# Kernel tuning notes

Hardware: AMD Instinct MI355X
Metric: run time of the kernel (lower is better)

The kernel has to match this reference:

```python
import jax, jax.numpy as jnp
from jax import lax
import numpy as np

V, H, D, B, W = 256, 512, 2, 256, 256  # vector_size, hidden_size, depth, batch, window_size


def setup_inputs() -> dict:
    key = jax.random.key(0)
    ks = jax.random.split(key, 13)
    scale = 0.04  # ~ 1/sqrt(hidden)
    names = ["w_ih_ltr", "w_hh_ltr", "b_ih_ltr", "b_hh_ltr", "w_fc_ltr", "b_fc_ltr",
             "w_ih_rtl", "w_hh_rtl", "b_ih_rtl", "b_hh_rtl", "w_fc_rtl", "b_fc_rtl"]
    shapes = [(D, 4 * H, V), (D, 4 * H, H), (D, 4 * H), (D, 4 * H), (D, V, H), (D, V)] * 2
    inp = {"x": jax.random.normal(ks[0], (B, W, V), dtype=jnp.float32)}
    for i, (n, s) in enumerate(zip(names, shapes)):
        inp[n] = jax.random.normal(ks[i + 1], s, dtype=jnp.float32) * scale
    return inp


def _lstm_cell(x, h, c, wih, whh, bih, bhh):
    # PyTorch gate order: i, f, g, o
    g = x @ wih.T + bih + h @ whh.T + bhh
    i, f, gg, o = jnp.split(g, 4, axis=-1)
    c = jax.nn.sigmoid(f) * c + jax.nn.sigmoid(i) * jnp.tanh(gg)
    h = jax.nn.sigmoid(o) * jnp.tanh(c)
    return h, c


def _run_dir(xs, wih, whh, bih, bhh, wfc, bfc):
    # xs: (T, B, V); depth LSTM(1-step)+FC blocks with persistent (h,c) per depth
    depth = wih.shape[0]
    h0 = jnp.zeros((depth, xs.shape[1], whh.shape[-1]), xs.dtype)

    def step(carry, x):
        h, c = carry
        v = x
        hs, cs = [], []
        for j in range(depth):  # small fixed depth loop
            hj, cj = _lstm_cell(v, h[j], c[j], wih[j], whh[j], bih[j], bhh[j])
            v = hj @ wfc[j].T + bfc[j]
            hs.append(hj)
            cs.append(cj)
        return (jnp.stack(hs), jnp.stack(cs)), v

    _, ys = lax.scan(step, (h0, h0), xs)
    return ys  # (T, B, V)


def reference(x, w_ih_ltr, w_hh_ltr, b_ih_ltr, b_hh_ltr, w_fc_ltr, b_fc_ltr,
              w_ih_rtl, w_hh_rtl, b_ih_rtl, b_hh_rtl, w_fc_rtl, b_fc_rtl):
    Wlen = x.shape[1]
    xs_f = jnp.swapaxes(x[:, :Wlen - 1, :], 0, 1)        # steps i = 0 .. W-2
    xs_b = jnp.swapaxes(x[:, Wlen - 1:0:-1, :], 0, 1)    # steps -(i+1) = W-1 .. 1
    ys_f = _run_dir(xs_f, w_ih_ltr, w_hh_ltr, b_ih_ltr, b_hh_ltr, w_fc_ltr, b_fc_ltr)
    ys_b = _run_dir(xs_b, w_ih_rtl, w_hh_rtl, b_ih_rtl, b_hh_rtl, w_fc_rtl, b_fc_rtl)
    # torch.stack(output, dim=1): forward outputs then backward outputs -> (B, 2*(W-1), V)
    return jnp.swapaxes(jnp.concatenate([ys_f, ys_b], axis=0), 0, 1)
```

## Files before the change

kernel.cpp:

```cpp
#include <hip/hip_runtime.h>
#include <hip/hip_bf16.h>

using bf16   = __bf16;
using bf16x8 = __attribute__((ext_vector_type(8))) __bf16;
using f32x4  = __attribute__((ext_vector_type(4))) float;
using u32x4  = __attribute__((ext_vector_type(4))) unsigned int;

#define TSTEPS 255
#define UNITE  512
#define HPAR   (16*16*512)
#define WA_UNITS_DIR (128*24)
#define WB_UNITS_DIR (128*32)
#define WC_UNITS_DIR (16*16)

#define MFMA(acc, a, b) acc = __builtin_amdgcn_mfma_f32_16x16x32_bf16((a), (b), (acc), 0, 0, 0)

__device__ __forceinline__ float sigmoidf_(float x) { return 1.f / (1.f + __expf(-x)); }
__device__ __forceinline__ float tanhf_(float x) {
    float e = __expf(-2.f * fabsf(x));
    float t = (1.f - e) / (1.f + e);
    return copysignf(t, x);
}

__device__ __forceinline__ void storeh_coh(bf16* ph, bf16* pl,
                                           unsigned short vh, unsigned short vl) {
    asm volatile(
        "global_store_short %0, %2, off sc0 sc1\n\t"
        "global_store_short %1, %3, off sc0 sc1"
        :: "v"(ph), "v"(pl), "v"(vh), "v"(vl)
        : "memory");
}

__device__ __forceinline__ void stage32k(const bf16* gh, const bf16* gl,
                                         bf16* lds, int tid) {
    u32x4 a0, a1, a2, a3, b0, b1, b2, b3;
    const bf16* p0 = gh + tid * 8;
    const bf16* p1 = p0 + 2048;
    const bf16* p2 = p0 + 4096;
    const bf16* p3 = p0 + 6144;
    const bf16* q0 = gl + tid * 8;
    const bf16* q1 = q0 + 2048;
    const bf16* q2 = q0 + 4096;
    const bf16* q3 = q0 + 6144;
    asm volatile(
        "global_load_dwordx4 %0, %8, off sc0 sc1\n\t"
        "global_load_dwordx4 %1, %9, off sc0 sc1\n\t"
        "global_load_dwordx4 %2, %10, off sc0 sc1\n\t"
        "global_load_dwordx4 %3, %11, off sc0 sc1\n\t"
        "global_load_dwordx4 %4, %12, off sc0 sc1\n\t"
        "global_load_dwordx4 %5, %13, off sc0 sc1\n\t"
        "global_load_dwordx4 %6, %14, off sc0 sc1\n\t"
        "global_load_dwordx4 %7, %15, off sc0 sc1\n\t"
        "s_waitcnt vmcnt(0)"
        : "=&v"(a0), "=&v"(a1), "=&v"(a2), "=&v"(a3),
          "=&v"(b0), "=&v"(b1), "=&v"(b2), "=&v"(b3)
        : "v"(p0), "v"(p1), "v"(p2), "v"(p3),
          "v"(q0), "v"(q1), "v"(q2), "v"(q3)
        : "memory");
    *(u32x4*)(lds + tid * 8)                 = a0;
    *(u32x4*)(lds + tid * 8 + 2048)          = a1;
    *(u32x4*)(lds + tid * 8 + 4096)          = a2;
    *(u32x4*)(lds + tid * 8 + 6144)          = a3;
    *(u32x4*)(lds + 8192 + tid * 8)          = b0;
    *(u32x4*)(lds + 8192 + tid * 8 + 2048)   = b1;
    *(u32x4*)(lds + 8192 + tid * 8 + 4096)   = b2;
    *(u32x4*)(lds + 8192 + tid * 8 + 6144)   = b3;
}

__device__ __forceinline__ void split_store8(const float* __restrict__ src,
                                             bf16* __restrict__ dh, bf16* __restrict__ dl) {
    float f[8];
    *(float4*)f       = *(const float4*)src;
    *(float4*)(f + 4) = *(const float4*)(src + 4);
    bf16x8 oh, ol;
    #pragma unroll
    for (int j = 0; j < 8; ++j) { bf16 h = (bf16)f[j]; oh[j] = h; ol[j] = (bf16)(f[j] - (float)h); }
    *(bf16x8*)dh = oh; *(bf16x8*)dl = ol;
}

__device__ __forceinline__ void gbarrier(unsigned* __restrict__ flags, int bid, unsigned epoch) {
    asm volatile("s_waitcnt vmcnt(0)" ::: "memory");
    __syncthreads();
    if (threadIdx.x == 0)
        asm volatile("global_store_dword %0, %1, off sc0 sc1"
                     :: "v"(&flags[bid]), "v"(epoch) : "memory");
    if (threadIdx.x < 64) {
        const int l = threadIdx.x;
        for (;;) {
            unsigned f0 = __hip_atomic_load(&flags[l],       __ATOMIC_RELAXED, __HIP_MEMORY_SCOPE_AGENT);
            unsigned f1 = __hip_atomic_load(&flags[l + 64],  __ATOMIC_RELAXED, __HIP_MEMORY_SCOPE_AGENT);
            unsigned f2 = __hip_atomic_load(&flags[l + 128], __ATOMIC_RELAXED, __HIP_MEMORY_SCOPE_AGENT);
            unsigned f3 = __hip_atomic_load(&flags[l + 192], __ATOMIC_RELAXED, __HIP_MEMORY_SCOPE_AGENT);
            if (__all(f0 >= epoch && f1 >= epoch && f2 >= epoch && f3 >= epoch)) break;
            __builtin_amdgcn_s_sleep(1);
        }
    }
    __syncthreads();
}


__global__ void k_pack_wa(const float* __restrict__ wihL, const float* __restrict__ whhL,
                          const float* __restrict__ wihR, const float* __restrict__ whhR,
                          bf16* __restrict__ wah, bf16* __restrict__ wal) {
    int gid = blockIdx.x * 256 + threadIdx.x;
    int lane = gid & 63, u = gid >> 6;
    int kb = u % 24; int tn = (u / 24) & 127; int dir = u / 3072;
    int r = lane & 15, q = lane >> 4;
    int n = tn * 16 + r, k = kb * 32 + q * 8;
    const float* wih = dir ? wihR : wihL;
    const float* whh = dir ? whhR : whhL;
    const float* src = (k < 256) ? (wih + (size_t)n * 256 + k)
                                 : (whh + (size_t)n * 512 + (k - 256));
    split_store8(src, wah + (size_t)u * UNITE + lane * 8, wal + (size_t)u * UNITE + lane * 8);
}

__global__ void k_wcomb(const float* __restrict__ wihL, const float* __restrict__ wfcL,
                        const float* __restrict__ wihR, const float* __restrict__ wfcR,
                        float* __restrict__ wcf) {
    size_t gid = (size_t)blockIdx.x * 256 + threadIdx.x;
    int k = gid & 511; int n = (gid >> 9) & 2047; int dir = (int)(gid >> 20);
    const float* wih1 = (dir ? wihR : wihL) + (size_t)2048 * 256;
    const float* wfc0 = (dir ? wfcR : wfcL);
    float s = 0.f;
    #pragma unroll 8
    for (int v = 0; v < 256; ++v)
        s = fmaf(wih1[(size_t)n * 256 + v], wfc0[(size_t)v * 512 + k], s);
    wcf[gid] = s;
}

__global__ void k_pack_wb(const float* __restrict__ whhL, const float* __restrict__ whhR,
                          const float* __restrict__ wcf,
                          bf16* __restrict__ wbh, bf16* __restrict__ wbl) {
    int gid = blockIdx.x * 256 + threadIdx.x;
    int lane = gid & 63, u = gid >> 6;
    int kb = u & 31, tn = (u >> 5) & 127, dir = u >> 12;
    int r = lane & 15, q = lane >> 4;
    int n = tn * 16 + r, k = kb * 32 + q * 8;
    const float* src;
    if (k < 512) {
        src = wcf + ((size_t)dir * 2048 + n) * 512 + k;
    } else {
        const float* whh1 = (dir ? whhR : whhL) + (size_t)2048 * 512;
        src = whh1 + (size_t)n * 512 + (k - 512);
    }
    split_store8(src, wbh + (size_t)u * UNITE + lane * 8, wbl + (size_t)u * UNITE + lane * 8);
}

__global__ void k_pack_wc(const float* __restrict__ wfcL, const float* __restrict__ wfcR,
                          bf16* __restrict__ wch, bf16* __restrict__ wcl) {
    int gid = blockIdx.x * 256 + threadIdx.x;
    int lane = gid & 63, u = gid >> 6;
    int kb = u & 15, tn = (u >> 4) & 15, dir = u >> 8;
    int r = lane & 15, q = lane >> 4;
    int n = tn * 16 + r, k = kb * 32 + q * 8;
    const float* wfc1 = (dir ? wfcR : wfcL) + (size_t)256 * 512;
    split_store8(wfc1 + (size_t)n * 512 + k,
                 wch + (size_t)u * UNITE + lane * 8, wcl + (size_t)u * UNITE + lane * 8);
}

__global__ void k_bias(const float* __restrict__ bihL, const float* __restrict__ bhhL,
                       const float* __restrict__ bfcL, const float* __restrict__ wihL,
                       const float* __restrict__ bihR, const float* __restrict__ bhhR,
                       const float* __restrict__ bfcR, const float* __restrict__ wihR,
                       float* __restrict__ ba, float* __restrict__ bb, float* __restrict__ bc) {
    int gid = blockIdx.x * 256 + threadIdx.x;
    int n = gid & 2047, dir = gid >> 11;
    const float* bih = dir ? bihR : bihL;
    const float* bhh = dir ? bhhR : bhhL;
    const float* bfc = dir ? bfcR : bfcL;
    const float* wih1 = (dir ? wihR : wihL) + (size_t)2048 * 256;
    ba[dir * 2048 + n] = bih[n] + bhh[n];
    float s = bih[2048 + n] + bhh[2048 + n];
    #pragma unroll 8
    for (int v = 0; v < 256; ++v)
        s = fmaf(bfc[v], wih1[(size_t)n * 256 + v], s);
    bb[dir * 2048 + n] = s;
    if (n < 256) bc[dir * 256 + n] = bfc[256 + n];
}

__global__ __launch_bounds__(256) void bilstm_main(
    const float* __restrict__ x,
    const bf16* __restrict__ wah, const bf16* __restrict__ wal,
    const bf16* __restrict__ wbh, const bf16* __restrict__ wbl,
    const bf16* __restrict__ wch, const bf16* __restrict__ wcl,
    bf16* __restrict__ h0pk, bf16* __restrict__ h1pk,
    const float* __restrict__ ba, const float* __restrict__ bb,
    const float* __restrict__ bc, float* __restrict__ out,
    unsigned* __restrict__ flags)
{
    const int bid  = blockIdx.x;
    const int nslc = bid & 7;
    const int bq   = (bid >> 3) & 15;
    const int dir  = bid >> 7;
    const int tid  = threadIdx.x;
    const int wv   = tid >> 6;
    const int lane = tid & 63;
    const int r = lane & 15, q = lane >> 4;

    __shared__ __align__(16) bf16 h0s[16384];
    __shared__ __align__(16) bf16 h1s[16384];

    const bf16* WAh = wah + (size_t)dir * WA_UNITS_DIR * UNITE;
    const bf16* WAl = wal + (size_t)dir * WA_UNITS_DIR * UNITE;
    const bf16* WBh = wbh + (size_t)dir * WB_UNITS_DIR * UNITE;
    const bf16* WBl = wbl + (size_t)dir * WB_UNITS_DIR * UNITE;
    const bf16* WCh = wch + (size_t)dir * WC_UNITS_DIR * UNITE;
    const bf16* WCl = wcl + (size_t)dir * WC_UNITS_DIR * UNITE;
    bf16* H0 = h0pk + (size_t)dir * 4 * HPAR;
    bf16* H1 = h1pk + (size_t)dir * 4 * HPAR;
    const float* BA = ba + dir * 2048;
    const float* BB = bb + dir * 2048;
    const float* BC = bc + dir * 256;

    const int nbase = nslc * 4 + wv;
    const int col   = nslc * 64 + wv * 16 + r;
    const float bia0 = BA[col], bia1 = BA[512 + col], bia2 = BA[1024 + col], bia3 = BA[1536 + col];
    const float bib0 = BB[col], bib1 = BB[512 + col], bib2 = BB[1024 + col], bib3 = BB[1536 + col];

    const int hunit  = bq * 16 + nslc * 2 + (wv >> 1);
    const int hw_off = ((wv & 1) * 2 + (r >> 3)) * 128 + q * 32 + (r & 7);

    const int tn  = nslc * 2 + (wv & 1);
    const float byc = BC[tn * 16 + r];

    f32x4 c0 = {0.f, 0.f, 0.f, 0.f}, c1 = {0.f, 0.f, 0.f, 0.f};
    unsigned epoch = 0;

    #pragma unroll
    for (int k2 = 0; k2 < 8; ++k2) *(u32x4*)(h0s + tid * 8 + k2 * 2048) = (u32x4){0, 0, 0, 0};
    __syncthreads();

    for (int t = 0; t <= TSTEPS; ++t) {
        const int pw = t & 1, pr = pw ^ 1;
        stage32k(H1 + (size_t)pr * 2 * HPAR + (size_t)bq * 8192,
                 H1 + (size_t)pr * 2 * HPAR + HPAR + (size_t)bq * 8192, h1s, tid);
        if (t < TSTEPS) {
            const int pos = dir ? (255 - t) : t;
            f32x4 acc[4] = {{0,0,0,0},{0,0,0,0},{0,0,0,0},{0,0,0,0}};
            const float* xp = x + ((size_t)(bq * 16 + r) * 256 + pos) * 256 + q * 8;
            #pragma unroll
            for (int kb = 0; kb < 8; ++kb) {
                float xf[8];
                *(float4*)xf       = *(const float4*)(xp + kb * 32);
                *(float4*)(xf + 4) = *(const float4*)(xp + kb * 32 + 4);
                bf16x8 axh, axl;
                #pragma unroll
                for (int j = 0; j < 8; ++j) { bf16 h = (bf16)xf[j]; axh[j] = h; axl[j] = (bf16)(xf[j] - (float)h); }
                #pragma unroll
                for (int g = 0; g < 4; ++g) {
                    const size_t wu = ((size_t)((g * 32 + nbase) * 24 + kb)) * UNITE + lane * 8;
                    bf16x8 bh = *(const bf16x8*)(WAh + wu);
                    bf16x8 bl = *(const bf16x8*)(WAl + wu);
                    MFMA(acc[g], axh, bh); MFMA(acc[g], axh, bl); MFMA(acc[g], axl, bh);
                }
            }
            #pragma unroll
            for (int hk = 0; hk < 16; ++hk) {
                bf16x8 ah = *(const bf16x8*)(h0s + hk * 512 + lane * 8);
                bf16x8 al = *(const bf16x8*)(h0s + 8192 + hk * 512 + lane * 8);
                #pragma unroll
                for (int g = 0; g < 4; ++g) {
                    const size_t wu = ((size_t)((g * 32 + nbase) * 24 + 8 + hk)) * UNITE + lane * 8;
                    bf16x8 bh = *(const bf16x8*)(WAh + wu);
                    bf16x8 bl = *(const bf16x8*)(WAl + wu);
                    MFMA(acc[g], ah, bh); MFMA(acc[g], ah, bl); MFMA(acc[g], al, bh);
                }
            }
            bf16* WH = H0 + (size_t)pw * 2 * HPAR + (size_t)hunit * 512 + hw_off;
            bf16* WL = WH + HPAR;
            #pragma unroll
            for (int i = 0; i < 4; ++i) {
                float gi = sigmoidf_(acc[0][i] + bia0);
                float gf = sigmoidf_(acc[1][i] + bia1);
                float gg = tanhf_   (acc[2][i] + bia2);
                float go = sigmoidf_(acc[3][i] + bia3);
                float cc = gf * c0[i] + gi * gg;
                c0[i] = cc;
                float hv = go * tanhf_(cc);
                bf16 hh = (bf16)hv;
                bf16 hl = (bf16)(hv - (float)hh);
                storeh_coh(WH + i * 8, WL + i * 8,
                           __builtin_bit_cast(unsigned short, hh),
                           __builtin_bit_cast(unsigned short, hl));
            }
        }
        __syncthreads();
        if (t >= 1 && wv < 2) {
            f32x4 accy = {0, 0, 0, 0};
            #pragma unroll
            for (int kb = 0; kb < 16; ++kb) {
                bf16x8 ah = *(const bf16x8*)(h1s + kb * 512 + lane * 8);
                bf16x8 al = *(const bf16x8*)(h1s + 8192 + kb * 512 + lane * 8);
                const size_t wu = ((size_t)(tn * 16 + kb)) * UNITE + lane * 8;
                bf16x8 bh = *(const bf16x8*)(WCh + wu);
                bf16x8 bl = *(const bf16x8*)(WCl + wu);
                MFMA(accy, ah, bh); MFMA(accy, ah, bl); MFMA(accy, al, bh);
            }
            const int tout = dir ? (255 + (t - 1)) : (t - 1);
            #pragma unroll
            for (int i = 0; i < 4; ++i)
                out[((size_t)(bq * 16 + 4 * q + i) * 510 + tout) * 256 + tn * 16 + r] = accy[i] + byc;
        }
        ++epoch; gbarrier(flags, bid, epoch);
        if (t < TSTEPS) {
            stage32k(H0 + (size_t)pw * 2 * HPAR + (size_t)bq * 8192,
                     H0 + (size_t)pw * 2 * HPAR + HPAR + (size_t)bq * 8192, h0s, tid);
            __syncthreads();
            f32x4 acc[4] = {{0,0,0,0},{0,0,0,0},{0,0,0,0},{0,0,0,0}};
            #pragma unroll
            for (int hk = 0; hk < 16; ++hk) {
                bf16x8 ah = *(const bf16x8*)(h0s + hk * 512 + lane * 8);
                bf16x8 al = *(const bf16x8*)(h0s + 8192 + hk * 512 + lane * 8);
                #pragma unroll
                for (int g = 0; g < 4; ++g) {
                    const size_t wu = ((size_t)((g * 32 + nbase) * 32 + hk)) * UNITE + lane * 8;
                    bf16x8 bh = *(const bf16x8*)(WBh + wu);
                    bf16x8 bl = *(const bf16x8*)(WBl + wu);
                    MFMA(acc[g], ah, bh); MFMA(acc[g], ah, bl); MFMA(acc[g], al, bh);
                }
            }
            #pragma unroll
            for (int hk = 0; hk < 16; ++hk) {
                bf16x8 ah = *(const bf16x8*)(h1s + hk * 512 + lane * 8);
                bf16x8 al = *(const bf16x8*)(h1s + 8192 + hk * 512 + lane * 8);
                #pragma unroll
                for (int g = 0; g < 4; ++g) {
                    const size_t wu = ((size_t)((g * 32 + nbase) * 32 + 16 + hk)) * UNITE + lane * 8;
                    bf16x8 bh = *(const bf16x8*)(WBh + wu);
                    bf16x8 bl = *(const bf16x8*)(WBl + wu);
                    MFMA(acc[g], ah, bh); MFMA(acc[g], ah, bl); MFMA(acc[g], al, bh);
                }
            }
            bf16* WH = H1 + (size_t)pw * 2 * HPAR + (size_t)hunit * 512 + hw_off;
            bf16* WL = WH + HPAR;
            #pragma unroll
            for (int i = 0; i < 4; ++i) {
                float gi = sigmoidf_(acc[0][i] + bib0);
                float gf = sigmoidf_(acc[1][i] + bib1);
                float gg = tanhf_   (acc[2][i] + bib2);
                float go = sigmoidf_(acc[3][i] + bib3);
                float cc = gf * c1[i] + gi * gg;
                c1[i] = cc;
                float hv = go * tanhf_(cc);
                bf16 hh = (bf16)hv;
                bf16 hl = (bf16)(hv - (float)hh);
                storeh_coh(WH + i * 8, WL + i * 8,
                           __builtin_bit_cast(unsigned short, hh),
                           __builtin_bit_cast(unsigned short, hl));
            }
        }
        ++epoch; gbarrier(flags, bid, epoch);
    }
}

extern "C" void kernel_launch(void* const* d_in, const int* in_sizes, int n_in,
                              void* d_out, int out_size, void* d_ws, size_t ws_size,
                              hipStream_t stream) {
    (void)in_sizes; (void)n_in; (void)ws_size;
    const float* x    = (const float*)d_in[0];
    const float* wihL = (const float*)d_in[1];
    const float* whhL = (const float*)d_in[2];
    const float* bihL = (const float*)d_in[3];
    const float* bhhL = (const float*)d_in[4];
    const float* wfcL = (const float*)d_in[5];
    const float* bfcL = (const float*)d_in[6];
    const float* wihR = (const float*)d_in[7];
    const float* whhR = (const float*)d_in[8];
    const float* bihR = (const float*)d_in[9];
    const float* bhhR = (const float*)d_in[10];
    const float* wfcR = (const float*)d_in[11];
    const float* bfcR = (const float*)d_in[12];

    char* ws = (char*)d_ws;
    size_t off = 0;
    auto take = [&](size_t bytes) -> char* {
        off = (off + 255) & ~(size_t)255;
        char* p = ws + off;
        off += bytes;
        return p;
    };
    bf16*     WAH = (bf16*)take((size_t)2 * WA_UNITS_DIR * 1024);
    bf16*     WAL = (bf16*)take((size_t)2 * WA_UNITS_DIR * 1024);
    bf16*     WBH = (bf16*)take((size_t)2 * WB_UNITS_DIR * 1024);
    bf16*     WBL = (bf16*)take((size_t)2 * WB_UNITS_DIR * 1024);
    bf16*     WCH = (bf16*)take((size_t)2 * WC_UNITS_DIR * 1024);
    bf16*     WCL = (bf16*)take((size_t)2 * WC_UNITS_DIR * 1024);
    bf16*     H0  = (bf16*)take((size_t)8 * HPAR * 2);
    bf16*     H1  = (bf16*)take((size_t)8 * HPAR * 2);
    float*    WCF = (float*)take((size_t)2 * 2048 * 512 * 4);
    float*    BA  = (float*)take((size_t)2 * 2048 * 4);
    float*    BB  = (float*)take((size_t)2 * 2048 * 4);
    float*    BC  = (float*)take((size_t)2 * 256 * 4);
    unsigned* FLG = (unsigned*)take((size_t)256 * 4);

    hipMemsetAsync(H0, 0, (size_t)8 * HPAR * 2, stream);
    hipMemsetAsync(H1, 0, (size_t)8 * HPAR * 2, stream);
    hipMemsetAsync(FLG, 0, (size_t)256 * 4, stream);
    hipMemsetAsync(d_out, 0, (size_t)out_size * 4, stream);

    k_pack_wa<<<1536, 256, 0, stream>>>(wihL, whhL, wihR, whhR, WAH, WAL);
    k_wcomb  <<<8192, 256, 0, stream>>>(wihL, wfcL, wihR, wfcR, WCF);
    k_pack_wb<<<2048, 256, 0, stream>>>(whhL, whhR, WCF, WBH, WBL);
    k_pack_wc<<<128,  256, 0, stream>>>(wfcL, wfcR, WCH, WCL);
    k_bias   <<<16,   256, 0, stream>>>(bihL, bhhL, bfcL, wihL, bihR, bhhR, bfcR, wihR, BA, BB, BC);

    bilstm_main<<<256, 256, 0, stream>>>(x, WAH, WAL, WBH, WBL, WCH, WCL,
                                         H0, H1, BA, BB, BC, (float*)d_out, FLG);
}
```

Measured before the change: 32.24 ms.

## Split K reduction across two wave groups with 512-thread blocks

Doubles the threads per block of the persistent BiLSTM kernel from 256 to 512. The K dimension of each gate GEMM is split between two groups of four waves, and the partial sums are combined through shared-memory buffers. The output FC GEMM is split the same way across four waves, and the h-state staging loads are spread over the larger block. This aims to shorten the serial per-timestep MFMA chain on the critical path, at the cost of extra __syncthreads, LDS traffic and register pressure under the 512-thread launch bound.

```diff
diff --git a/kernel.cpp b/kernel.cpp
--- a/kernel.cpp
+++ b/kernel.cpp
@@ -31,40 +31,26 @@
         : "memory");
 }
 
-__device__ __forceinline__ void stage32k(const bf16* gh, const bf16* gl,
-                                         bf16* lds, int tid) {
-    u32x4 a0, a1, a2, a3, b0, b1, b2, b3;
+__device__ __forceinline__ void stage32k_512(const bf16* gh, const bf16* gl,
+                                             bf16* lds, int tid) {
+    u32x4 a0, a1, b0, b1;
     const bf16* p0 = gh + tid * 8;
-    const bf16* p1 = p0 + 2048;
-    const bf16* p2 = p0 + 4096;
-    const bf16* p3 = p0 + 6144;
+    const bf16* p1 = p0 + 4096;
     const bf16* q0 = gl + tid * 8;
-    const bf16* q1 = q0 + 2048;
-    const bf16* q2 = q0 + 4096;
-    const bf16* q3 = q0 + 6144;
+    const bf16* q1 = q0 + 4096;
     asm volatile(
-        "global_load_dwordx4 %0, %8, off sc0 sc1\n\t"
-        "global_load_dwordx4 %1, %9, off sc0 sc1\n\t"
-        "global_load_dwordx4 %2, %10, off sc0 sc1\n\t"
-        "global_load_dwordx4 %3, %11, off sc0 sc1\n\t"
-        "global_load_dwordx4 %4, %12, off sc0 sc1\n\t"
-        "global_load_dwordx4 %5, %13, off sc0 sc1\n\t"
-        "global_load_dwordx4 %6, %14, off sc0 sc1\n\t"
-        "global_load_dwordx4 %7, %15, off sc0 sc1\n\t"
+        "global_load_dwordx4 %0, %4, off sc0 sc1\n\t"
+        "global_load_dwordx4 %1, %5, off sc0 sc1\n\t"
+        "global_load_dwordx4 %2, %6, off sc0 sc1\n\t"
+        "global_load_dwordx4 %3, %7, off sc0 sc1\n\t"
         "s_waitcnt vmcnt(0)"
-        : "=&v"(a0), "=&v"(a1), "=&v"(a2), "=&v"(a3),
-          "=&v"(b0), "=&v"(b1), "=&v"(b2), "=&v"(b3)
-        : "v"(p0), "v"(p1), "v"(p2), "v"(p3),
-          "v"(q0), "v"(q1), "v"(q2), "v"(q3)
+        : "=&v"(a0), "=&v"(a1), "=&v"(b0), "=&v"(b1)
+        : "v"(p0), "v"(p1), "v"(q0), "v"(q1)
         : "memory");
-    *(u32x4*)(lds + tid * 8)                 = a0;
-    *(u32x4*)(lds + tid * 8 + 2048)          = a1;
-    *(u32x4*)(lds + tid * 8 + 4096)          = a2;
-    *(u32x4*)(lds + tid * 8 + 6144)          = a3;
-    *(u32x4*)(lds + 8192 + tid * 8)          = b0;
-    *(u32x4*)(lds + 8192 + tid * 8 + 2048)   = b1;
-    *(u32x4*)(lds + 8192 + tid * 8 + 4096)   = b2;
-    *(u32x4*)(lds + 8192 + tid * 8 + 6144)   = b3;
+    *(u32x4*)(lds + tid * 8)               = a0;
+    *(u32x4*)(lds + tid * 8 + 4096)        = a1;
+    *(u32x4*)(lds + 8192 + tid * 8)        = b0;
+    *(u32x4*)(lds + 8192 + tid * 8 + 4096) = b1;
 }
 
 __device__ __forceinline__ void split_store8(const float* __restrict__ src,
@@ -178,7 +164,7 @@
     if (n < 256) bc[dir * 256 + n] = bfc[256 + n];
 }
 
-__global__ __launch_bounds__(256) void bilstm_main(
+__global__ __launch_bounds__(512) void bilstm_main(
     const float* __restrict__ x,
     const bf16* __restrict__ wah, const bf16* __restrict__ wal,
     const bf16* __restrict__ wbh, const bf16* __restrict__ wbl,
@@ -194,11 +180,15 @@
     const int dir  = bid >> 7;
     const int tid  = threadIdx.x;
     const int wv   = tid >> 6;
+    const int wq   = wv & 3;
+    const int kg   = wv >> 2;
     const int lane = tid & 63;
     const int r = lane & 15, q = lane >> 4;
 
     __shared__ __align__(16) bf16 h0s[16384];
     __shared__ __align__(16) bf16 h1s[16384];
+    __shared__ __align__(16) float gred[4][4][64][4];
+    __shared__ __align__(16) float yred[2][64][4];
 
     const bf16* WAh = wah + (size_t)dir * WA_UNITS_DIR * UNITE;
     const bf16* WAl = wal + (size_t)dir * WA_UNITS_DIR * UNITE;
@@ -212,68 +202,88 @@
     const float* BB = bb + dir * 2048;
     const float* BC = bc + dir * 256;
 
-    const int nbase = nslc * 4 + wv;
-    const int col   = nslc * 64 + wv * 16 + r;
+    const int nbase = nslc * 4 + wq;
+    const int col   = nslc * 64 + wq * 16 + r;
     const float bia0 = BA[col], bia1 = BA[512 + col], bia2 = BA[1024 + col], bia3 = BA[1536 + col];
     const float bib0 = BB[col], bib1 = BB[512 + col], bib2 = BB[1024 + col], bib3 = BB[1536 + col];
 
-    const int hunit  = bq * 16 + nslc * 2 + (wv >> 1);
-    const int hw_off = ((wv & 1) * 2 + (r >> 3)) * 128 + q * 32 + (r & 7);
-
-    const int tn  = nslc * 2 + (wv & 1);
+    const int hunit  = bq * 16 + nslc * 2 + (wq >> 1);
+    const int hw_off = ((wq & 1) * 2 + (r >> 3)) * 128 + q * 32 + (r & 7);
+
+    const int tn  = nslc * 2 + (wq & 1);
     const float byc = BC[tn * 16 + r];
 
     f32x4 c0 = {0.f, 0.f, 0.f, 0.f}, c1 = {0.f, 0.f, 0.f, 0.f};
     unsigned epoch = 0;
 
     #pragma unroll
-    for (int k2 = 0; k2 < 8; ++k2) *(u32x4*)(h0s + tid * 8 + k2 * 2048) = (u32x4){0, 0, 0, 0};
+    for (int k2 = 0; k2 < 4; ++k2) *(u32x4*)(h0s + tid * 8 + k2 * 4096) = (u32x4){0, 0, 0, 0};
     __syncthreads();
 
     for (int t = 0; t <= TSTEPS; ++t) {
         const int pw = t & 1, pr = pw ^ 1;
-        stage32k(H1 + (size_t)pr * 2 * HPAR + (size_t)bq * 8192,
-                 H1 + (size_t)pr * 2 * HPAR + HPAR + (size_t)bq * 8192, h1s, tid);
+        stage32k_512(H1 + (size_t)pr * 2 * HPAR + (size_t)bq * 8192,
+                     H1 + (size_t)pr * 2 * HPAR + HPAR + (size_t)bq * 8192, h1s, tid);
+        f32x4 acc[4] = {{0,0,0,0},{0,0,0,0},{0,0,0,0},{0,0,0,0}};
         if (t < TSTEPS) {
-            const int pos = dir ? (255 - t) : t;
-            f32x4 acc[4] = {{0,0,0,0},{0,0,0,0},{0,0,0,0},{0,0,0,0}};
-            const float* xp = x + ((size_t)(bq * 16 + r) * 256 + pos) * 256 + q * 8;
-            #pragma unroll
-            for (int kb = 0; kb < 8; ++kb) {
-                float xf[8];
-                *(float4*)xf       = *(const float4*)(xp + kb * 32);
-                *(float4*)(xf + 4) = *(const float4*)(xp + kb * 32 + 4);
-                bf16x8 axh, axl;
-                #pragma unroll
-                for (int j = 0; j < 8; ++j) { bf16 h = (bf16)xf[j]; axh[j] = h; axl[j] = (bf16)(xf[j] - (float)h); }
-                #pragma unroll
-                for (int g = 0; g < 4; ++g) {
-                    const size_t wu = ((size_t)((g * 32 + nbase) * 24 + kb)) * UNITE + lane * 8;
-                    bf16x8 bh = *(const bf16x8*)(WAh + wu);
-                    bf16x8 bl = *(const bf16x8*)(WAl + wu);
-                    MFMA(acc[g], axh, bh); MFMA(acc[g], axh, bl); MFMA(acc[g], axl, bh);
-                }
+            if (kg == 0) {
+                const int pos = dir ? (255 - t) : t;
+                const float* xp = x + ((size_t)(bq * 16 + r) * 256 + pos) * 256 + q * 8;
+                #pragma unroll
+                for (int kb = 0; kb < 8; ++kb) {
+                    float xf[8];
+                    *(float4*)xf       = *(const float4*)(xp + kb * 32);
+                    *(float4*)(xf + 4) = *(const float4*)(xp + kb * 32 + 4);
+                    bf16x8 axh, axl;
+                    #pragma unroll
+                    for (int j = 0; j < 8; ++j) { bf16 h = (bf16)xf[j]; axh[j] = h; axl[j] = (bf16)(xf[j] - (float)h); }
+                    #pragma unroll
+                    for (int g = 0; g < 4; ++g) {
+                        const size_t wu = ((size_t)((g * 32 + nbase) * 24 + kb)) * UNITE + lane * 8;
+                        bf16x8 bh = *(const bf16x8*)(WAh + wu);
+                        bf16x8 bl = *(const bf16x8*)(WAl + wu);
+                        MFMA(acc[g], axh, bh); MFMA(acc[g], axh, bl); MFMA(acc[g], axl, bh);
+                    }
+                }
+                #pragma unroll
+                for (int hk = 0; hk < 4; ++hk) {
+                    bf16x8 ah = *(const bf16x8*)(h0s + hk * 512 + lane * 8);
+                    bf16x8 al = *(const bf16x8*)(h0s + 8192 + hk * 512 + lane * 8);
+                    #pragma unroll
+                    for (int g = 0; g < 4; ++g) {
+                        const size_t wu = ((size_t)((g * 32 + nbase) * 24 + 8 + hk)) * UNITE + lane * 8;
+                        bf16x8 bh = *(const bf16x8*)(WAh + wu);
+                        bf16x8 bl = *(const bf16x8*)(WAl + wu);
+                        MFMA(acc[g], ah, bh); MFMA(acc[g], ah, bl); MFMA(acc[g], al, bh);
+                    }
+                }
+            } else {
+                #pragma unroll
+                for (int hk = 4; hk < 16; ++hk) {
+                    bf16x8 ah = *(const bf16x8*)(h0s + hk * 512 + lane * 8);
+                    bf16x8 al = *(const bf16x8*)(h0s + 8192 + hk * 512 + lane * 8);
+                    #pragma unroll
+                    for (int g = 0; g < 4; ++g) {
+                        const size_t wu = ((size_t)((g * 32 + nbase) * 24 + 8 + hk)) * UNITE + lane * 8;
+                        bf16x8 bh = *(const bf16x8*)(WAh + wu);
+                        bf16x8 bl = *(const bf16x8*)(WAl + wu);
+                        MFMA(acc[g], ah, bh); MFMA(acc[g], ah, bl); MFMA(acc[g], al, bh);
+                    }
+                }
+                #pragma unroll
+                for (int g = 0; g < 4; ++g) *(f32x4*)&gred[wq][g][lane][0] = acc[g];
             }
-            #pragma unroll
-            for (int hk = 0; hk < 16; ++hk) {
-                bf16x8 ah = *(const bf16x8*)(h0s + hk * 512 + lane * 8);
-                bf16x8 al = *(const bf16x8*)(h0s + 8192 + hk * 512 + lane * 8);
-                #pragma unroll
-                for (int g = 0; g < 4; ++g) {
-                    const size_t wu = ((size_t)((g * 32 + nbase) * 24 + 8 + hk)) * UNITE + lane * 8;
-                    bf16x8 bh = *(const bf16x8*)(WAh + wu);
-                    bf16x8 bl = *(const bf16x8*)(WAl + wu);
-                    MFMA(acc[g], ah, bh); MFMA(acc[g], ah, bl); MFMA(acc[g], al, bh);
-                }
-            }
+        }
+        __syncthreads();
+        if (t < TSTEPS && kg == 0) {
             bf16* WH = H0 + (size_t)pw * 2 * HPAR + (size_t)hunit * 512 + hw_off;
             bf16* WL = WH + HPAR;
             #pragma unroll
             for (int i = 0; i < 4; ++i) {
-                float gi = sigmoidf_(acc[0][i] + bia0);
-                float gf = sigmoidf_(acc[1][i] + bia1);
-                float gg = tanhf_   (acc[2][i] + bia2);
-                float go = sigmoidf_(acc[3][i] + bia3);
+                float gi = sigmoidf_(acc[0][i] + gred[wq][0][lane][i] + bia0);
+                float gf = sigmoidf_(acc[1][i] + gred[wq][1][lane][i] + bia1);
+                float gg = tanhf_   (acc[2][i] + gred[wq][2][lane][i] + bia2);
+                float go = sigmoidf_(acc[3][i] + gred[wq][3][lane][i] + bia3);
                 float cc = gf * c0[i] + gi * gg;
                 c0[i] = cc;
                 float hv = go * tanhf_(cc);
@@ -284,11 +294,12 @@
                            __builtin_bit_cast(unsigned short, hl));
             }
         }
-        __syncthreads();
-        if (t >= 1 && wv < 2) {
-            f32x4 accy = {0, 0, 0, 0};
+        f32x4 accy = {0, 0, 0, 0};
+        if (t >= 1 && kg == 1) {
+            const int kb0 = (wq >> 1) * 8;
             #pragma unroll
-            for (int kb = 0; kb < 16; ++kb) {
+            for (int kk = 0; kk < 8; ++kk) {
+                const int kb = kb0 + kk;
                 bf16x8 ah = *(const bf16x8*)(h1s + kb * 512 + lane * 8);
                 bf16x8 al = *(const bf16x8*)(h1s + 8192 + kb * 512 + lane * 8);
                 const size_t wu = ((size_t)(tn * 16 + kb)) * UNITE + lane * 8;
@@ -296,57 +307,70 @@
                 bf16x8 bl = *(const bf16x8*)(WCl + wu);
                 MFMA(accy, ah, bh); MFMA(accy, ah, bl); MFMA(accy, al, bh);
             }
+            if (wq >= 2) *(f32x4*)&yred[wq & 1][lane][0] = accy;
+        }
+        __syncthreads();
+        if (t >= 1 && kg == 1 && wq < 2) {
             const int tout = dir ? (255 + (t - 1)) : (t - 1);
             #pragma unroll
             for (int i = 0; i < 4; ++i)
-                out[((size_t)(bq * 16 + 4 * q + i) * 510 + tout) * 256 + tn * 16 + r] = accy[i] + byc;
+                out[((size_t)(bq * 16 + 4 * q + i) * 510 + tout) * 256 + tn * 16 + r]
+                    = accy[i] + yred[wq][lane][i] + byc;
         }
         ++epoch; gbarrier(flags, bid, epoch);
         if (t < TSTEPS) {
-            stage32k(H0 + (size_t)pw * 2 * HPAR + (size_t)bq * 8192,
-                     H0 + (size_t)pw * 2 * HPAR + HPAR + (size_t)bq * 8192, h0s, tid);
+            stage32k_512(H0 + (size_t)pw * 2 * HPAR + (size_t)bq * 8192,
+                         H0 + (size_t)pw * 2 * HPAR + HPAR + (size_t)bq * 8192, h0s, tid);
             __syncthreads();
-            f32x4 acc[4] = {{0,0,0,0},{0,0,0,0},{0,0,0,0},{0,0,0,0}};
-            #pragma unroll
-            for (int hk = 0; hk < 16; ++hk) {
-                bf16x8 ah = *(const bf16x8*)(h0s + hk * 512 + lane * 8);
-                bf16x8 al = *(const bf16x8*)(h0s + 8192 + hk * 512 + lane * 8);
-                #pragma unroll
-                for (int g = 0; g < 4; ++g) {
-                    const size_t wu = ((size_t)((g * 32 + nbase) * 32 + hk)) * UNITE + lane * 8;
-                    bf16x8 bh = *(const bf16x8*)(WBh + wu);
-                    bf16x8 bl = *(const bf16x8*)(WBl + wu);
-                    MFMA(acc[g], ah, bh); MFMA(acc[g], ah, bl); MFMA(acc[g], al, bh);
-                }
+            f32x4 accb[4] = {{0,0,0,0},{0,0,0,0},{0,0,0,0},{0,0,0,0}};
+            if (kg == 0) {
+                #pragma unroll
+                for (int hk = 0; hk < 16; ++hk) {
+                    bf16x8 ah = *(const bf16x8*)(h0s + hk * 512 + lane * 8);
+                    bf16x8 al = *(const bf16x8*)(h0s + 8192 + hk * 512 + lane * 8);
+                    #pragma unroll
+                    for (int g = 0; g < 4; ++g) {
+                        const size_t wu = ((size_t)((g * 32 + nbase) * 32 + hk)) * UNITE + lane * 8;
+                        bf16x8 bh = *(const bf16x8*)(WBh + wu);
+                        bf16x8 bl = *(const bf16x8*)(WBl + wu);
+                        MFMA(accb[g], ah, bh); MFMA(accb[g], ah, bl); MFMA(accb[g], al, bh);
+                    }
+                }
+            } else {
+                #pragma unroll
+                for (int hk = 0; hk < 16; ++hk) {
+                    bf16x8 ah = *(const bf16x8*)(h1s + hk * 512 + lane * 8);
+                    bf16x8 al = *(const bf16x8*)(h1s + 8192 + hk * 512 + lane * 8);
+                    #pragma unroll
+                    for (int g = 0; g < 4; ++g) {
+                        const size_t wu = ((size_t)((g * 32 + nbase) * 32 + 16 + hk)) * UNITE + lane * 8;
+                        bf16x8 bh = *(const bf16x8*)(WBh + wu);
+                        bf16x8 bl = *(const bf16x8*)(WBl + wu);
+                        MFMA(accb[g], ah, bh); MFMA(accb[g], ah, bl); MFMA(accb[g], al, bh);
+                    }
+                }
+                #pragma unroll
+                for (int g = 0; g < 4; ++g) *(f32x4*)&gred[wq][g][lane][0] = accb[g];
             }
-            #pragma unroll
-            for (int hk = 0; hk < 16; ++hk) {
-                bf16x8 ah = *(const bf16x8*)(h1s + hk * 512 + lane * 8);
-                bf16x8 al = *(const bf16x8*)(h1s + 8192 + hk * 512 + lane * 8);
-                #pragma unroll
-                for (int g = 0; g < 4; ++g) {
-                    const size_t wu = ((size_t)((g * 32 + nbase) * 32 + 16 + hk)) * UNITE + lane * 8;
-                    bf16x8 bh = *(const bf16x8*)(WBh + wu);
-                    bf16x8 bl = *(const bf16x8*)(WBl + wu);
-                    MFMA(acc[g], ah, bh); MFMA(acc[g], ah, bl); MFMA(acc[g], al, bh);
-                }
-            }
-            bf16* WH = H1 + (size_t)pw * 2 * HPAR + (size_t)hunit * 512 + hw_off;
-            bf16* WL = WH + HPAR;
-            #pragma unroll
-            for (int i = 0; i < 4; ++i) {
-                float gi = sigmoidf_(acc[0][i] + bib0);
-                float gf = sigmoidf_(acc[1][i] + bib1);
-                float gg = tanhf_   (acc[2][i] + bib2);
-                float go = sigmoidf_(acc[3][i] + bib3);
-                float cc = gf * c1[i] + gi * gg;
-                c1[i] = cc;
-                float hv = go * tanhf_(cc);
-                bf16 hh = (bf16)hv;
-                bf16 hl = (bf16)(hv - (float)hh);
-                storeh_coh(WH + i * 8, WL + i * 8,
-                           __builtin_bit_cast(unsigned short, hh),
-                           __builtin_bit_cast(unsigned short, hl));
+            __syncthreads();
+            if (kg == 0) {
+                bf16* WH = H1 + (size_t)pw * 2 * HPAR + (size_t)hunit * 512 + hw_off;
+                bf16* WL = WH + HPAR;
+                #pragma unroll
+                for (int i = 0; i < 4; ++i) {
+                    float gi = sigmoidf_(accb[0][i] + gred[wq][0][lane][i] + bib0);
+                    float gf = sigmoidf_(accb[1][i] + gred[wq][1][lane][i] + bib1);
+                    float gg = tanhf_   (accb[2][i] + gred[wq][2][lane][i] + bib2);
+                    float go = sigmoidf_(accb[3][i] + gred[wq][3][lane][i] + bib3);
+                    float cc = gf * c1[i] + gi * gg;
+                    c1[i] = cc;
+                    float hv = go * tanhf_(cc);
+                    bf16 hh = (bf16)hv;
+                    bf16 hl = (bf16)(hv - (float)hh);
+                    storeh_coh(WH + i * 8, WL + i * 8,
+                               __builtin_bit_cast(unsigned short, hh),
+                               __builtin_bit_cast(unsigned short, hl));
+                }
             }
         }
         ++epoch; gbarrier(flags, bid, epoch);
@@ -404,6 +428,6 @@
     k_pack_wc<<<128,  256, 0, stream>>>(wfcL, wfcR, WCH, WCL);
     k_bias   <<<16,   256, 0, stream>>>(bihL, bhhL, bfcL, wihL, bihR, bhhR, bfcR, wihR, BA, BB, BC);
 
-    bilstm_main<<<256, 256, 0, stream>>>(x, WAH, WAL, WBH, WBL, WCH, WCL,
+    bilstm_main<<<256, 512, 0, stream>>>(x, WAH, WAL, WBH, WBL, WCH, WCL,
                                          H0, H1, BA, BB, BC, (float*)d_out, FLG);
 }
```

Measured after the change: 28.55 ms. 1.13x faster.
